# Optimization experiments

Measured on AMD Instinct MI355X. Metric: run time of the kernel, lower is better.

## Reference

```python
import jax, jax.numpy as jnp
import numpy as np

B = 64          # batch of trees
L = 10          # gated internal levels below the root
H = 256         # hidden_size
E = 256         # embed_size
V = 64          # embedding vocab (relation/role types)
TOTAL = 2 ** (L + 1) - 2   # heap layout: level i (1..L) has 2^i nodes at offset 2^i - 2


def setup_inputs() -> dict:
    key = jax.random.key(0)
    k = jax.random.split(key, 7)
    s = 0.05
    return {
        "node_ids": jax.random.randint(k[0], (B, TOTAL), 0, V, dtype=jnp.int32),
        "emb_table": jax.random.normal(k[1], (V, E), jnp.float32) * s,
        # W: x-projections, order (forget, input, output, update)
        "W": jax.random.normal(k[2], (4, E, H), jnp.float32) * s,
        "bW": jax.random.normal(k[3], (4, H), jnp.float32) * s,
        # U: hidden projections, [gate, child] with gate order
        # (forget_left, forget_right, input, output, update), child order (left, right)
        "U": jax.random.normal(k[4], (5, 2, H, H), jnp.float32) * s,
        "Ws": jax.random.normal(k[5], (2 * H, 3), jnp.float32) * s,
        "bs": jax.random.normal(k[6], (3,), jnp.float32) * s,
    }


def _tree_lstm(node_ids, emb_table, W, bW, U, Ws, bs):
    Bn, total = node_ids.shape
    Lv = int(np.log2(total + 2)) - 1          # number of gated levels (static)
    Hh = U.shape[-1]
    # Wforget is shared by both forget gates (as in the original module)
    gate_map = jnp.array([0, 0, 1, 2, 3])      # x-projection index per gate
    h = c = None
    for lev in range(Lv, 0, -1):               # leaves-up level order
        n = 2 ** lev
        off = 2 ** lev - 2
        ids = node_ids[:, off:off + n]         # [B, n]
        x = emb_table[ids]                     # [B, n, E]
        xg = jnp.einsum('bne,geh->gbnh', x, W) + bW[:, None, None, :]  # [4,B,n,H]
        if h is None:
            # deepest level: children are leaves -> zero h and c (init_hidden())
            hl = hr = cl = cr = jnp.zeros((Bn, n, Hh), x.dtype)
        else:
            hl, hr = h[:, 0::2], h[:, 1::2]
            cl, cr = c[:, 0::2], c[:, 1::2]
        pre = (jnp.einsum('bnh,ghk->gbnk', hl, U[:, 0])
               + jnp.einsum('bnh,ghk->gbnk', hr, U[:, 1])
               + xg[gate_map])                 # [5,B,n,H]
        f_l = jax.nn.sigmoid(pre[0])
        f_r = jax.nn.sigmoid(pre[1])
        i_g = jax.nn.sigmoid(pre[2])
        o_g = jax.nn.sigmoid(pre[3])
        u_g = jnp.tanh(pre[4])
        c = i_g * u_g + f_l * cl + f_r * cr
        h = o_g * jnp.tanh(c)
    # root: concatenate the two children's hidden states, then score
    root_hidden = jnp.concatenate([h[:, 0], h[:, 1]], axis=-1)   # [B, 2H]
    scores = root_hidden @ Ws + bs                               # [B, 3]
    return scores, root_hidden


def reference(node_ids, emb_table, W, bW, U, Ws, bs):
    return _tree_lstm(node_ids, emb_table, W, bW, U, Ws, bs)
```

## Files before the change

kernel.cpp:

```cpp
#include <hip/hip_runtime.h>
#include <hip/hip_bf16.h>
#include <stdint.h>
#include <math.h>


typedef __bf16 bf16x8 __attribute__((ext_vector_type(8)));
typedef float  f32x4  __attribute__((ext_vector_type(4)));
typedef int    i32x4  __attribute__((ext_vector_type(4)));

__device__ __forceinline__ float sigf(float x) { return 1.f / (1.f + __expf(-x)); }
__device__ __forceinline__ float tanhfast(float x) {
    return 1.f - 2.f / (__expf(2.f * x) + 1.f);
}

__global__ void xg_prep(const float* __restrict__ emb, const float* __restrict__ W,
                        const float* __restrict__ bW, float* __restrict__ xg) {
    int g = blockIdx.x >> 6, v = blockIdx.x & 63, k = threadIdx.x;
    __shared__ float e[256];
    e[k] = emb[v * 256 + k];
    __syncthreads();
    float s = bW[g * 256 + k];
    const float* Wg = W + g * 65536 + k;
#pragma unroll 4
    for (int i = 0; i < 256; i++) s += e[i] * Wg[i * 256];
    xg[(g * 64 + v) * 256 + k] = s;
}

__global__ void bt_prep(const float* __restrict__ U, __bf16* __restrict__ BtP) {
    int t = blockIdx.x * 256 + threadIdx.x;
    int g    = t >> 14;
    int r    = t & 16383;
    int ct   = r >> 10;
    int ks   = (r >> 6) & 15;
    int lane = t & 63;
    int lr = lane & 15, q = lane >> 4;
    int col = ct * 16 + lr;
    int kbase = ks * 32 + q * 8;
    bf16x8 v8;
#pragma unroll
    for (int e = 0; e < 8; e++) {
        int k = kbase + e;
        int s = k >> 8, kk = k & 255;
        v8[e] = (__bf16)U[((g * 2 + s) * 256 + kk) * 256 + col];
    }
    *(bf16x8*)(BtP + (long)t * 8) = v8;
}

__global__ void leaf_kernel(const int* __restrict__ ids, const float* __restrict__ xg,
                            __bf16* __restrict__ h, __bf16* __restrict__ c) {
    int col = threadIdx.x;
    int r0 = blockIdx.x * 32;
    for (int r = r0; r < r0 + 32; r++) {
        int b = r >> 10, j = r & 1023;
        int id = ids[b * 2046 + 1022 + j];
        float x1 = xg[(64  + id) * 256 + col];
        float x2 = xg[(128 + id) * 256 + col];
        float x3 = xg[(192 + id) * 256 + col];
        float ig = sigf(x1);
        float og = sigf(x2);
        float ug = tanhfast(x3);
        float cv = ig * ug;
        float hv = og * tanhfast(cv);
        h[r * 256 + col] = (__bf16)hv;
        c[r * 256 + col] = (__bf16)cv;
    }
}

__global__ __launch_bounds__(512, 2) void level_kernel(
    const __bf16* __restrict__ A, const __bf16* __restrict__ Cprev,
    const __bf16* __restrict__ BtP, const float* __restrict__ xg,
    const int* __restrict__ ids, __bf16* __restrict__ h_out,
    __bf16* __restrict__ c_out, float* __restrict__ rh_out, int lev, int M, int RG) {
    __shared__ __bf16 Blds[5 * 16 * 512];
    const int gid = blockIdx.x;
    int rg, ct;
    if ((RG & 7) == 0) {
        int xcd = gid & 7;
        int t   = gid >> 3;
        ct = t & 15;
        rg = ((t >> 4) << 3) | xcd;
    } else {
        rg = gid >> 4;
        ct = gid & 15;
    }
    const int tid  = threadIdx.x;
    const int wave = tid >> 6;
    const int lane = tid & 63;
    const int lr = lane & 15, q = lane >> 4;
    const long wrow = (long)rg * 512 + wave * 64;
    const bool active = (wrow < M);

#pragma unroll
    for (int i = 0; i < 10; i++) {
        int c = tid + i * 512;
        int g = c >> 10;
        int r = c & 1023;
        i32x4 v = *(const i32x4*)(BtP + (long)(g * 16 + ct) * 8192 + r * 8);
        *(i32x4*)(&Blds[g * 8192 + r * 8]) = v;
    }

    const __bf16* Ap = A + (wrow + lr) * 512 + q * 8;
    bf16x8 af[3][4];
    if (active) {
#pragma unroll
        for (int mt = 0; mt < 4; mt++) {
            af[0][mt] = *(const bf16x8*)(Ap + mt * 8192);
            af[1][mt] = *(const bf16x8*)(Ap + mt * 8192 + 32);
        }
    }

    __syncthreads();

    const int n = 1 << lev;
    const int gcol = ct * 16 + lr;
    int idv[4][4];
    __bf16 clv[4][4], crv[4][4];
    if (active) {
#pragma unroll
        for (int mt = 0; mt < 4; mt++)
#pragma unroll
            for (int v = 0; v < 4; v++) {
                long grow = wrow + mt * 16 + q * 4 + v;
                int b = (int)(grow >> lev);
                int j = (int)(grow & (n - 1));
                idv[mt][v] = ids[b * 2046 + (n - 2) + j];
                clv[mt][v] = Cprev[grow * 512 + gcol];
                crv[mt][v] = Cprev[grow * 512 + 256 + gcol];
            }
    }

    if (active) {
        f32x4 acc[5][4];
#pragma unroll
        for (int g2 = 0; g2 < 5; g2++)
#pragma unroll
            for (int mt = 0; mt < 4; mt++) acc[g2][mt] = (f32x4){0.f, 0.f, 0.f, 0.f};

        bf16x8 bb[2][5];
#pragma unroll
        for (int g2 = 0; g2 < 5; g2++)
            bb[0][g2] = *(const bf16x8*)(&Blds[g2 * 8192 + lane * 8]);

#pragma unroll
        for (int s = 0; s < 16; s++) {
            if (s + 1 < 16) {
#pragma unroll
                for (int g2 = 0; g2 < 5; g2++)
                    bb[(s + 1) & 1][g2] =
                        *(const bf16x8*)(&Blds[g2 * 8192 + (s + 1) * 512 + lane * 8]);
            }
            if (s + 2 < 16) {
#pragma unroll
                for (int mt = 0; mt < 4; mt++)
                    af[(s + 2) % 3][mt] =
                        *(const bf16x8*)(Ap + mt * 8192 + (s + 2) * 32);
            }
#pragma unroll
            for (int g2 = 0; g2 < 5; g2++)
#pragma unroll
                for (int mt = 0; mt < 4; mt++)
                    acc[g2][mt] = __builtin_amdgcn_mfma_f32_16x16x32_bf16(
                        af[s % 3][mt], bb[s & 1][g2], acc[g2][mt], 0, 0, 0);
        }

#pragma unroll
        for (int mt = 0; mt < 4; mt++) {
#pragma unroll
            for (int v = 0; v < 4; v++) {
                long grow = wrow + mt * 16 + q * 4 + v;
                const float* xp = xg + idv[mt][v] * 256 + gcol;
                float fl = sigf(acc[0][mt][v] + xp[0]);
                float fr = sigf(acc[1][mt][v] + xp[0]);
                float ig = sigf(acc[2][mt][v] + xp[16384]);
                float og = sigf(acc[3][mt][v] + xp[32768]);
                float ug = tanhfast(acc[4][mt][v] + xp[49152]);
                float cv = ig * ug + fl * (float)clv[mt][v] + fr * (float)crv[mt][v];
                float hv = og * tanhfast(cv);
                h_out[grow * 256 + gcol] = (__bf16)hv;
                c_out[grow * 256 + gcol] = (__bf16)cv;
                if (rh_out) rh_out[grow * 256 + gcol] = hv;
            }
        }
    }
}

__global__ void scores_kernel(const float* __restrict__ rh, const float* __restrict__ Ws,
                              const float* __restrict__ bs, float* __restrict__ out) {
    int b = blockIdx.x;
    int t = threadIdx.x >> 6, lane = threadIdx.x & 63;
    float s = 0.f;
    for (int i = lane; i < 512; i += 64) s += rh[b * 512 + i] * Ws[i * 3 + t];
    for (int o = 32; o > 0; o >>= 1) s += __shfl_down(s, o);
    if (lane == 0) out[b * 3 + t] = s + bs[t];
}

extern "C" void kernel_launch(void* const* d_in, const int* in_sizes, int n_in,
                              void* d_out, int out_size, void* d_ws, size_t ws_size,
                              hipStream_t stream) {
    const int*   ids = (const int*)  d_in[0];
    const float* emb = (const float*)d_in[1];
    const float* W   = (const float*)d_in[2];
    const float* bW  = (const float*)d_in[3];
    const float* U   = (const float*)d_in[4];
    const float* Ws  = (const float*)d_in[5];
    const float* bs  = (const float*)d_in[6];
    float* out = (float*)d_out;

    char* ws = (char*)d_ws;
    float*  xg  = (float*)ws;
    __bf16* BtP = (__bf16*)(ws + 262144);
    __bf16* h0  = (__bf16*)(ws + 1572864);
    __bf16* c0  = (__bf16*)(ws + 35127296);
    __bf16* h1  = (__bf16*)(ws + 68681728);
    __bf16* c1  = (__bf16*)(ws + 85458944);

    xg_prep<<<dim3(256), dim3(256), 0, stream>>>(emb, W, bW, xg);
    bt_prep<<<dim3(320), dim3(256), 0, stream>>>(U, BtP);
    leaf_kernel<<<dim3(2048), dim3(256), 0, stream>>>(ids, xg, h0, c0);

    __bf16* hb[2] = {h0, h1};
    __bf16* cb[2] = {c0, c1};
    int cur = 0;
    for (int lev = 9; lev >= 1; lev--) {
        int M = 64 << lev;
        int RG = (M + 511) / 512;
        float* rh = (lev == 1) ? (out + 192) : nullptr;
        level_kernel<<<dim3(RG * 16), dim3(512), 0, stream>>>(
            hb[cur], cb[cur], BtP, xg, ids, hb[1 - cur], cb[1 - cur], rh, lev, M, RG);
        cur = 1 - cur;
    }
    scores_kernel<<<dim3(64), dim3(192), 0, stream>>>(out + 192, Ws, bs, out);
}
```

Before: 449.5 us.

## Stream A fragments through LDS with async global_load_lds double buffering

Replaces the per-wave register prefetch of the A (child hidden) fragments with direct global-to-LDS loads into a per-wave double buffer, using explicit vmcnt/lgkmcnt waits. The aim is to overlap A loads with the MFMA chain and cut VGPR pressure from the triple-buffered register fragments. It also moves the Cprev and id gathers after the GEMM loop, converting them to float there. In exchange it adds 32KB of LDS per block, which may limit the two-blocks-per-CU target, and the hand-written waitcnt placement risks stalls or races.

```diff
diff --git a/kernel.cpp b/kernel.cpp
--- a/kernel.cpp
+++ b/kernel.cpp
@@ -66,12 +66,18 @@
     }
 }
 
+#define GLD_LDS(srcp, dstp) \
+    __builtin_amdgcn_global_load_lds( \
+        (const __attribute__((address_space(1))) uint32_t*)(srcp), \
+        (__attribute__((address_space(3))) uint32_t*)(dstp), 16, 0, 0)
+
 __global__ __launch_bounds__(512, 2) void level_kernel(
     const __bf16* __restrict__ A, const __bf16* __restrict__ Cprev,
     const __bf16* __restrict__ BtP, const float* __restrict__ xg,
     const int* __restrict__ ids, __bf16* __restrict__ h_out,
     __bf16* __restrict__ c_out, float* __restrict__ rh_out, int lev, int M, int RG) {
     __shared__ __bf16 Blds[5 * 16 * 512];
+    __shared__ __bf16 Alds[2][8][4][512];
     const int gid = blockIdx.x;
     int rg, ct;
     if ((RG & 7) == 0) {
@@ -99,23 +105,66 @@
         *(i32x4*)(&Blds[g * 8192 + r * 8]) = v;
     }
 
-    const __bf16* Ap = A + (wrow + lr) * 512 + q * 8;
-    bf16x8 af[3][4];
+    const __bf16* Asrc = A + (wrow + lr) * 512 + q * 8;
     if (active) {
 #pragma unroll
-        for (int mt = 0; mt < 4; mt++) {
-            af[0][mt] = *(const bf16x8*)(Ap + mt * 8192);
-            af[1][mt] = *(const bf16x8*)(Ap + mt * 8192 + 32);
+        for (int mt = 0; mt < 4; mt++)
+            GLD_LDS(Asrc + mt * 8192, &Alds[0][wave][mt][0]);
+    }
+
+    __syncthreads();
+
+    if (active) {
+#pragma unroll
+        for (int mt = 0; mt < 4; mt++)
+            GLD_LDS(Asrc + mt * 8192 + 32, &Alds[1][wave][mt][0]);
+
+        f32x4 acc[5][4];
+#pragma unroll
+        for (int g2 = 0; g2 < 5; g2++)
+#pragma unroll
+            for (int mt = 0; mt < 4; mt++) acc[g2][mt] = (f32x4){0.f, 0.f, 0.f, 0.f};
+
+        bf16x8 afr[2][4], bfr[2][5];
+#pragma unroll
+        for (int mt = 0; mt < 4; mt++)
+            afr[0][mt] = *(const bf16x8*)(&Alds[0][wave][mt][lane * 8]);
+#pragma unroll
+        for (int g2 = 0; g2 < 5; g2++)
+            bfr[0][g2] = *(const bf16x8*)(&Blds[g2 * 8192 + lane * 8]);
+
+#pragma unroll
+        for (int c = 0; c < 16; c++) {
+            const int cur = c & 1, nxt = cur ^ 1;
+            if (c + 1 < 16) {
+                asm volatile("s_waitcnt vmcnt(0)" ::: "memory");
+#pragma unroll
+                for (int mt = 0; mt < 4; mt++)
+                    afr[nxt][mt] = *(const bf16x8*)(&Alds[nxt][wave][mt][lane * 8]);
+#pragma unroll
+                for (int g2 = 0; g2 < 5; g2++)
+                    bfr[nxt][g2] =
+                        *(const bf16x8*)(&Blds[g2 * 8192 + (c + 1) * 512 + lane * 8]);
+                if (c + 2 < 16) {
+                    asm volatile("s_waitcnt lgkmcnt(9)" ::: "memory");
+#pragma unroll
+                    for (int mt = 0; mt < 4; mt++)
+                        GLD_LDS(Asrc + mt * 8192 + (c + 2) * 32,
+                                &Alds[cur][wave][mt][0]);
+                }
+            }
+#pragma unroll
+            for (int g2 = 0; g2 < 5; g2++)
+#pragma unroll
+                for (int mt = 0; mt < 4; mt++)
+                    acc[g2][mt] = __builtin_amdgcn_mfma_f32_16x16x32_bf16(
+                        afr[cur][mt], bfr[cur][g2], acc[g2][mt], 0, 0, 0);
         }
-    }
-
-    __syncthreads();
-
-    const int n = 1 << lev;
-    const int gcol = ct * 16 + lr;
-    int idv[4][4];
-    __bf16 clv[4][4], crv[4][4];
-    if (active) {
+
+        const int n = 1 << lev;
+        const int gcol = ct * 16 + lr;
+        int idv[4][4];
+        float clv[4][4], crv[4][4];
 #pragma unroll
         for (int mt = 0; mt < 4; mt++)
 #pragma unroll
@@ -124,45 +173,9 @@
                 int b = (int)(grow >> lev);
                 int j = (int)(grow & (n - 1));
                 idv[mt][v] = ids[b * 2046 + (n - 2) + j];
-                clv[mt][v] = Cprev[grow * 512 + gcol];
-                crv[mt][v] = Cprev[grow * 512 + 256 + gcol];
+                clv[mt][v] = (float)Cprev[grow * 512 + gcol];
+                crv[mt][v] = (float)Cprev[grow * 512 + 256 + gcol];
             }
-    }
-
-    if (active) {
-        f32x4 acc[5][4];
-#pragma unroll
-        for (int g2 = 0; g2 < 5; g2++)
-#pragma unroll
-            for (int mt = 0; mt < 4; mt++) acc[g2][mt] = (f32x4){0.f, 0.f, 0.f, 0.f};
-
-        bf16x8 bb[2][5];
-#pragma unroll
-        for (int g2 = 0; g2 < 5; g2++)
-            bb[0][g2] = *(const bf16x8*)(&Blds[g2 * 8192 + lane * 8]);
-
-#pragma unroll
-        for (int s = 0; s < 16; s++) {
-            if (s + 1 < 16) {
-#pragma unroll
-                for (int g2 = 0; g2 < 5; g2++)
-                    bb[(s + 1) & 1][g2] =
-                        *(const bf16x8*)(&Blds[g2 * 8192 + (s + 1) * 512 + lane * 8]);
-            }
-            if (s + 2 < 16) {
-#pragma unroll
-                for (int mt = 0; mt < 4; mt++)
-                    af[(s + 2) % 3][mt] =
-                        *(const bf16x8*)(Ap + mt * 8192 + (s + 2) * 32);
-            }
-#pragma unroll
-            for (int g2 = 0; g2 < 5; g2++)
-#pragma unroll
-                for (int mt = 0; mt < 4; mt++)
-                    acc[g2][mt] = __builtin_amdgcn_mfma_f32_16x16x32_bf16(
-                        af[s % 3][mt], bb[s & 1][g2], acc[g2][mt], 0, 0, 0);
-        }
-
 #pragma unroll
         for (int mt = 0; mt < 4; mt++) {
 #pragma unroll
@@ -174,7 +187,7 @@
                 float ig = sigf(acc[2][mt][v] + xp[16384]);
                 float og = sigf(acc[3][mt][v] + xp[32768]);
                 float ug = tanhfast(acc[4][mt][v] + xp[49152]);
-                float cv = ig * ug + fl * (float)clv[mt][v] + fr * (float)crv[mt][v];
+                float cv = ig * ug + fl * clv[mt][v] + fr * crv[mt][v];
                 float hv = og * tanhfast(cv);
                 h_out[grow * 256 + gcol] = (__bf16)hv;
                 c_out[grow * 256 + gcol] = (__bf16)cv;
```

After: 488.5 us. 8.7% more time.
